# Performance work log

Hardware: AMD Instinct MI355X
Metric: run time of the kernel (lower is better)

Reference implementation:

```python
import jax, jax.numpy as jnp
import numpy as np

H = 896          # hidden_size
S = H // 2       # split_size = 448
Q = 256          # quantisation
B = 16384        # batch (parallel sampling streams)


def setup_inputs() -> dict:
    key = jax.random.key(0)
    ks = jax.random.split(key, 16)
    sc = 0.02
    return {
        "prev_y": jax.random.uniform(ks[0], (B, 2), dtype=jnp.float32),
        "prev_hidden": jax.random.normal(ks[1], (B, H), dtype=jnp.float32),
        "current_coarse": jax.random.uniform(ks[2], (B, 1), dtype=jnp.float32),
        # torch Linear weights are [out_features, in_features]
        "R_w": sc * jax.random.normal(ks[3], (3 * H, H), dtype=jnp.float32),
        "Ic_w": sc * jax.random.normal(ks[4], (3 * S, 2), dtype=jnp.float32),
        "If_w": sc * jax.random.normal(ks[5], (3 * S, 3), dtype=jnp.float32),
        "bias_u": jnp.zeros((H,), jnp.float32),
        "bias_r": jnp.zeros((H,), jnp.float32),
        "bias_e": jnp.zeros((H,), jnp.float32),
        "O1_w": sc * jax.random.normal(ks[6], (S, S), dtype=jnp.float32),
        "O1_b": jnp.zeros((S,), jnp.float32),
        "O2_w": sc * jax.random.normal(ks[7], (Q, S), dtype=jnp.float32),
        "O2_b": jnp.zeros((Q,), jnp.float32),
        "O3_w": sc * jax.random.normal(ks[8], (S, S), dtype=jnp.float32),
        "O3_b": jnp.zeros((S,), jnp.float32),
        "O4_w": sc * jax.random.normal(ks[9], (Q, S), dtype=jnp.float32),
        "O4_b": jnp.zeros((Q,), jnp.float32),
    }


def reference(prev_y, prev_hidden, current_coarse,
              R_w, Ic_w, If_w, bias_u, bias_r, bias_e,
              O1_w, O1_b, O2_w, O2_b, O3_w, O3_b, O4_w, O4_b):
    # recurrent projection: [B,H] @ [H,3H] -> [B,3H]
    R_hidden = prev_hidden @ R_w.T
    R_u, R_r, R_e = jnp.split(R_hidden, 3, axis=1)

    # coarse input projection: [B,2] -> [B,3S]
    cproj = prev_y @ Ic_w.T
    Ic_u, Ic_r, Ic_e = jnp.split(cproj, 3, axis=1)

    # fine input projection: [B,3] -> [B,3S]
    fine_in = jnp.concatenate([prev_y, current_coarse], axis=1)
    fproj = fine_in @ If_w.T
    If_u, If_r, If_e = jnp.split(fproj, 3, axis=1)

    I_u = jnp.concatenate([Ic_u, If_u], axis=1)  # [B,H]
    I_r = jnp.concatenate([Ic_r, If_r], axis=1)
    I_e = jnp.concatenate([Ic_e, If_e], axis=1)

    u = jax.nn.sigmoid(R_u + I_u + bias_u)
    r = jax.nn.sigmoid(R_r + I_r + bias_r)
    e = jnp.tanh(r * R_e + I_e + bias_e)
    hidden = u * prev_hidden + (1.0 - u) * e  # [B,H]

    h_coarse, h_fine = jnp.split(hidden, 2, axis=1)  # [B,S] each
    out_coarse = jax.nn.relu(h_coarse @ O1_w.T + O1_b) @ O2_w.T + O2_b  # [B,Q]
    out_fine = jax.nn.relu(h_fine @ O3_w.T + O3_b) @ O4_w.T + O4_b      # [B,Q]
    return (out_coarse, out_fine, hidden)
```

## Files before the change

kernel.cpp:

```cpp
#include <hip/hip_runtime.h>
#include <hip/hip_bf16.h>
#include <cstdint>

#define BB 16384
#define HH 896
#define SS 448
#define QQ 256
#define NPAD 2816

typedef __attribute__((ext_vector_type(4))) float f32x4;
typedef __attribute__((ext_vector_type(8))) short bf16x8;

__device__ __forceinline__ short f2bf(float f){
  union { float f; uint32_t u; } x; x.f = f;
  uint32_t r = (x.u + 0x7fffu + ((x.u >> 16) & 1u)) >> 16;
  return (short)r;
}
__device__ __forceinline__ float bf2f(short b){
  union { uint32_t u; float f; } x; x.u = ((uint32_t)(uint16_t)b) << 16;
  return x.f;
}

__global__ __launch_bounds__(256)
void castall_kernel(const float* __restrict__ ph, short* __restrict__ Ah,
                    const float* __restrict__ Rw, short* __restrict__ Rwh,
                    const float* __restrict__ O1w, short* __restrict__ O1b,
                    const float* __restrict__ O3w, short* __restrict__ O3b,
                    const float* __restrict__ O2w, short* __restrict__ O2b,
                    const float* __restrict__ O4w, short* __restrict__ O4b)
{
  int u = blockIdx.x * 256 + threadIdx.x;
  auto cp4 = [](short* d, const float* s, int jd, int js){
    float4 v = reinterpret_cast<const float4*>(s)[js];
    short4 o; o.x = f2bf(v.x); o.y = f2bf(v.y); o.z = f2bf(v.z); o.w = f2bf(v.w);
    reinterpret_cast<short4*>(d)[jd] = o;
  };
  auto z4 = [](short* d, int jd){
    short4 o; o.x = 0; o.y = 0; o.z = 0; o.w = 0;
    reinterpret_cast<short4*>(d)[jd] = o;
  };
  if (u < 3670016) { cp4(Ah, ph, u, u); return; }
  u -= 3670016;
  if (u < 602112) { cp4(Rwh, Rw, u, u); return; }
  u -= 602112;
  if (u < 28672) { z4(Rwh, 602112 + u); return; }
  u -= 28672;
  if (u < 57344) { if (u < 50176) cp4(O1b, O1w, u, u); else z4(O1b, u); return; }
  u -= 57344;
  if (u < 57344) { if (u < 50176) cp4(O3b, O3w, u, u); else z4(O3b, u); return; }
  u -= 57344;
  if (u < 32768) {
    int r = u >> 7, c4 = u & 127;
    if (c4 < 112) cp4(O2b, O2w, u, r * 112 + c4); else z4(O2b, u);
    return;
  }
  u -= 32768;
  if (u < 32768) {
    int r = u >> 7, c4 = u & 127;
    if (c4 < 112) cp4(O4b, O4w, u, r * 112 + c4); else z4(O4b, u);
    return;
  }
}

template<int EP>
__global__ __launch_bounds__(512, 2)
void gemm256_bt(const short* __restrict__ A0p, const short* __restrict__ A1p, int lda,
                const short* __restrict__ B0p, const short* __restrict__ B1p, int ldb,
                void* __restrict__ C0p, void* __restrict__ C1p, int ldc,
                const float* __restrict__ bias0, const float* __restrict__ bias1, int nbias,
                int Nvalid, int K, int nbn)
{
  const short* A  = blockIdx.z ? A1p : A0p;
  const short* Bt = blockIdx.z ? B1p : B0p;
  void* Cv        = blockIdx.z ? C1p : C0p;
  const float* bias = blockIdx.z ? bias1 : bias0;

  __shared__ short smem[65536];
  const int tid = threadIdx.x;
  const int w  = tid >> 6, ln = tid & 63;
  const int wr = w >> 2,  wc = w & 3;
  const int lr = ln & 15;
  const int lg = ln >> 4;
  const int srow = ln >> 3;
  const int sgc  = (ln & 7) ^ srow;

  int wg = blockIdx.x;
  const int cpx = gridDim.x >> 3;
  wg = (wg & 7) * cpx + (wg >> 3);
  const int bm = wg / nbn, bn = wg - bm * nbn;
  const long m0 = (long)bm * 256, n0 = (long)bn * 256;

  f32x4 acc[8][4] = {};

  auto stage = [&](const short* __restrict__ src, int ld, long rbase, int k0,
                   int lbase , int h) {
#pragma unroll
    for (int i = 0; i < 2; ++i) {
      const int rloc = h * 128 + i * 64 + w * 8;
      const short* g = src + (rbase + rloc + srow) * (long)ld + k0 + sgc * 8;
      __builtin_amdgcn_global_load_lds(
          (const __attribute__((address_space(1))) void*)g,
          (__attribute__((address_space(3))) void*)&smem[lbase + rloc * 64],
          16, 0, 0);
    }
  };
  auto rd = [&](int lbase, int r, int ks) -> bf16x8 {
    const int gc = ks * 4 + lg;
    return *reinterpret_cast<const bf16x8*>(&smem[lbase + r * 64 + ((gc ^ (r & 7)) << 3)]);
  };

  const int NT = K >> 6;
  stage(A,  lda, m0, 0, 0,     0);
  stage(Bt, ldb, n0, 0, 32768, 0);
  stage(Bt, ldb, n0, 0, 32768, 1);
  stage(A,  lda, m0, 0, 0,     1);
  asm volatile("s_waitcnt vmcnt(2)" ::: "memory");
  __builtin_amdgcn_s_barrier();
  asm volatile("" ::: "memory");
  __builtin_amdgcn_sched_barrier(0);

  for (int j = 0; j < NT; ++j) {
    const int Ab = (j & 1) * 16384;
    const int Bb = 32768 + (j & 1) * 16384;
    const int An = ((j + 1) & 1) * 16384;
    const int Bn = 32768 + ((j + 1) & 1) * 16384;
    const bool pf = (j + 1 < NT);
    const int k1 = (j + 1) << 6;
    bf16x8 b[4][2];
#pragma unroll
    for (int q = 0; q < 4; ++q) {
      bf16x8 a[2][2];
#pragma unroll
      for (int dm = 0; dm < 2; ++dm)
#pragma unroll
        for (int ks = 0; ks < 2; ++ks)
          a[dm][ks] = rd(Ab, q * 64 + dm * 32 + wr * 16 + lr, ks);
      if (q == 0) {
#pragma unroll
        for (int n = 0; n < 4; ++n)
#pragma unroll
          for (int ks = 0; ks < 2; ++ks)
            b[n][ks] = rd(Bb, wc * 64 + n * 16 + lr, ks);
        if (pf) {
          stage(A,  lda, m0, k1, An, 0);
          stage(Bt, ldb, n0, k1, Bn, 0);
          stage(Bt, ldb, n0, k1, Bn, 1);
          stage(A,  lda, m0, k1, An, 1);
        }
      }
      asm volatile("s_waitcnt lgkmcnt(0)" ::: "memory");
      __builtin_amdgcn_sched_barrier(0);
      __builtin_amdgcn_s_setprio(1);
#pragma unroll
      for (int dm = 0; dm < 2; ++dm)
#pragma unroll
        for (int n = 0; n < 4; ++n)
#pragma unroll
          for (int ks = 0; ks < 2; ++ks)
            acc[2 * q + dm][n] = __builtin_amdgcn_mfma_f32_16x16x32_bf16(
                a[dm][ks], b[n][ks], acc[2 * q + dm][n], 0, 0, 0);
      __builtin_amdgcn_s_setprio(0);
      __builtin_amdgcn_sched_barrier(0);
      if (q == 1) {
        if (pf) asm volatile("s_waitcnt vmcnt(8)" ::: "memory");
        else    asm volatile("s_waitcnt vmcnt(0)" ::: "memory");
        __builtin_amdgcn_s_barrier();
        asm volatile("" ::: "memory");
        __builtin_amdgcn_sched_barrier(0);
      } else if (q == 3) {
        asm volatile("s_waitcnt vmcnt(2)" ::: "memory");
        __builtin_amdgcn_s_barrier();
        asm volatile("" ::: "memory");
        __builtin_amdgcn_sched_barrier(0);
      }
    }
  }

  if (EP == 2) {
    const int lc = ln & 15, rg = lg * 4;
#pragma unroll
    for (int n = 0; n < 4; ++n) {
      const long col = n0 + wc * 64 + n * 16 + lc;
      const float bv = bias[col];
#pragma unroll
      for (int m = 0; m < 8; ++m) {
        const long row = m0 + m * 32 + wr * 16 + rg;
#pragma unroll
        for (int reg = 0; reg < 4; ++reg)
          ((float*)Cv)[(row + reg) * (long)ldc + col] = acc[m][n][reg] + bv;
      }
    }
    return;
  }

#pragma unroll
  for (int n = 0; n < 4; ++n) {
    const int col = wc * 64 + n * 16 + lr;
    float bv = 0.f;
    if (EP == 1) {
      const long gcol = n0 + col;
      bv = (gcol < nbias) ? bias[gcol] : 0.f;
    }
#pragma unroll
    for (int m = 0; m < 8; ++m) {
      const int row = m * 32 + wr * 16 + lg * 4;
#pragma unroll
      for (int reg = 0; reg < 4; ++reg) {
        float v = acc[m][n][reg];
        if (EP == 1) { v += bv; v = v > 0.f ? v : 0.f; }
        smem[(row + reg) * 256 + col] = f2bf(v);
      }
    }
  }
  __builtin_amdgcn_s_barrier();
  const int rt = tid >> 5;
  const int ct = (tid & 31) * 8;
  const long colg = n0 + ct;
  if (colg < Nvalid) {
#pragma unroll
    for (int p = 0; p < 16; ++p) {
      const int row = p * 16 + rt;
      bf16x8 v = *reinterpret_cast<const bf16x8*>(&smem[row * 256 + ct]);
      *reinterpret_cast<bf16x8*>(&((short*)Cv)[(m0 + row) * (long)ldc + colg]) = v;
    }
  }
}

__global__ __launch_bounds__(256)
void gates_kernel(const float* __restrict__ prev_y,
                  const short* __restrict__ Ah,
                  const float* __restrict__ ccoarse,
                  const float* __restrict__ Icw,
                  const float* __restrict__ Ifw,
                  const float* __restrict__ bu,
                  const float* __restrict__ br,
                  const float* __restrict__ be,
                  const short* __restrict__ Rh,
                  float* __restrict__ hid_out,
                  short* __restrict__ hid_bf)
{
  const int v = blockIdx.x * 256 + threadIdx.x;
  const int b = v / 112;
  const int h0 = (v - b * 112) * 8;
  const long rbase = (long)b * (3 * HH);

  const bf16x8 ru8 = *reinterpret_cast<const bf16x8*>(Rh + rbase + h0);
  const bf16x8 rr8 = *reinterpret_cast<const bf16x8*>(Rh + rbase + HH + h0);
  const bf16x8 re8 = *reinterpret_cast<const bf16x8*>(Rh + rbase + 2 * HH + h0);
  const bf16x8 ah8 = *reinterpret_cast<const bf16x8*>(Ah + (long)b * HH + h0);
  const float py0 = prev_y[2 * b], py1 = prev_y[2 * b + 1], c0 = ccoarse[b];

  float iu[8], ir[8], ie[8];
  if (h0 < SS) {
    const float4* cu = reinterpret_cast<const float4*>(Icw + 2 * h0);
    const float4* cr = reinterpret_cast<const float4*>(Icw + 2 * (SS + h0));
    const float4* ce = reinterpret_cast<const float4*>(Icw + 2 * (2 * SS + h0));
#pragma unroll
    for (int q = 0; q < 4; ++q) {
      float4 a = cu[q]; iu[2*q] = py0*a.x + py1*a.y; iu[2*q+1] = py0*a.z + py1*a.w;
      float4 r = cr[q]; ir[2*q] = py0*r.x + py1*r.y; ir[2*q+1] = py0*r.z + py1*r.w;
      float4 e = ce[q]; ie[2*q] = py0*e.x + py1*e.y; ie[2*q+1] = py0*e.z + py1*e.w;
    }
  } else {
    const int j0 = h0 - SS;
    const float* fu = Ifw + 3 * j0;
    const float* fr = Ifw + 3 * (SS + j0);
    const float* fe = Ifw + 3 * (2 * SS + j0);
#pragma unroll
    for (int j = 0; j < 8; ++j) {
      iu[j] = py0 * fu[3*j] + py1 * fu[3*j+1] + c0 * fu[3*j+2];
      ir[j] = py0 * fr[3*j] + py1 * fr[3*j+1] + c0 * fr[3*j+2];
      ie[j] = py0 * fe[3*j] + py1 * fe[3*j+1] + c0 * fe[3*j+2];
    }
  }
  const float4* bu4 = reinterpret_cast<const float4*>(bu + h0);
  const float4* br4 = reinterpret_cast<const float4*>(br + h0);
  const float4* be4 = reinterpret_cast<const float4*>(be + h0);
  float buv[8], brv[8], bev[8];
  { float4 a = bu4[0], b2 = bu4[1];
    buv[0]=a.x; buv[1]=a.y; buv[2]=a.z; buv[3]=a.w; buv[4]=b2.x; buv[5]=b2.y; buv[6]=b2.z; buv[7]=b2.w; }
  { float4 a = br4[0], b2 = br4[1];
    brv[0]=a.x; brv[1]=a.y; brv[2]=a.z; brv[3]=a.w; brv[4]=b2.x; brv[5]=b2.y; brv[6]=b2.z; brv[7]=b2.w; }
  { float4 a = be4[0], b2 = be4[1];
    bev[0]=a.x; bev[1]=a.y; bev[2]=a.z; bev[3]=a.w; bev[4]=b2.x; bev[5]=b2.y; bev[6]=b2.z; bev[7]=b2.w; }

  float hd[8];
  bf16x8 hb;
#pragma unroll
  for (int j = 0; j < 8; ++j) {
    float u = 1.f / (1.f + __expf(-(bf2f(ru8[j]) + iu[j] + buv[j])));
    float r = 1.f / (1.f + __expf(-(bf2f(rr8[j]) + ir[j] + brv[j])));
    float e = tanhf(r * bf2f(re8[j]) + ie[j] + bev[j]);
    hd[j] = u * bf2f(ah8[j]) + (1.f - u) * e;
    hb[j] = f2bf(hd[j]);
  }
  float4* ho = reinterpret_cast<float4*>(hid_out + (long)b * HH + h0);
  ho[0] = make_float4(hd[0], hd[1], hd[2], hd[3]);
  ho[1] = make_float4(hd[4], hd[5], hd[6], hd[7]);
  *reinterpret_cast<bf16x8*>(hid_bf + (long)b * HH + h0) = hb;
}

extern "C" void kernel_launch(void* const* d_in, const int* in_sizes, int n_in,
                              void* d_out, int out_size, void* d_ws, size_t ws_size,
                              hipStream_t stream)
{
  (void)in_sizes; (void)n_in; (void)out_size; (void)ws_size;
  const float* prev_y      = (const float*)d_in[0];
  const float* prev_hidden = (const float*)d_in[1];
  const float* ccoarse     = (const float*)d_in[2];
  const float* R_w  = (const float*)d_in[3];
  const float* Ic_w = (const float*)d_in[4];
  const float* If_w = (const float*)d_in[5];
  const float* bu   = (const float*)d_in[6];
  const float* br   = (const float*)d_in[7];
  const float* be   = (const float*)d_in[8];
  const float* O1w  = (const float*)d_in[9];
  const float* O1b  = (const float*)d_in[10];
  const float* O2w  = (const float*)d_in[11];
  const float* O2b  = (const float*)d_in[12];
  const float* O3w  = (const float*)d_in[13];
  const float* O3b  = (const float*)d_in[14];
  const float* O4w  = (const float*)d_in[15];
  const float* O4b  = (const float*)d_in[16];

  float* out_coarse = (float*)d_out;
  float* out_fine   = out_coarse + (long)BB * QQ;
  float* hidden     = out_fine + (long)BB * QQ;

  char* ws = (char*)d_ws;
  short* Ah   = (short*)(ws + 0);
  short* Rwh  = (short*)(ws + 29360128);
  short* Rh   = (short*)(ws + 34406400);
  short* hidb = (short*)(ws + 122486784);
  short* O1wb = (short*)(ws + 151846912);
  short* O3wb = (short*)(ws + 152305664);
  short* O2wb = (short*)(ws + 152764416);
  short* O4wb = (short*)(ws + 153026560);
  short* t1   = (short*)(ws + 0);
  short* t2   = (short*)(ws + 16777216);

  castall_kernel<<<17504, 256, 0, stream>>>(prev_hidden, Ah, R_w, Rwh,
                                            O1w, O1wb, O3w, O3wb, O2w, O2wb, O4w, O4wb);

  gemm256_bt<0><<<dim3(704, 1, 1), 512, 0, stream>>>(
      Ah, Ah, HH, Rwh, Rwh, HH, Rh, Rh, 3 * HH,
      nullptr, nullptr, 0, 3 * HH, HH, NPAD / 256);

  gates_kernel<<<BB * 112 / 256, 256, 0, stream>>>(prev_y, Ah, ccoarse,
                                                   Ic_w, If_w, bu, br, be, Rh, hidden, hidb);

  gemm256_bt<1><<<dim3(128, 1, 2), 512, 0, stream>>>(
      hidb, hidb + 448, HH, O1wb, O3wb, 448, t1, t2, 512,
      O1b, O3b, 448, 512, 448, 2);

  gemm256_bt<2><<<dim3(64, 1, 2), 512, 0, stream>>>(
      t1, t2, 512, O2wb, O4wb, 512, out_coarse, out_fine, QQ,
      O2b, O4b, QQ, QQ, 512, 1);
}
```

Measured before the change: 214.8 us.

## Restructure GEMM main loop into two phases and swizzle epilogue LDS staging

```diff
diff --git a/kernel.cpp b/kernel.cpp
--- a/kernel.cpp
+++ b/kernel.cpp
@@ -117,7 +117,6 @@
   asm volatile("s_waitcnt vmcnt(2)" ::: "memory");
   __builtin_amdgcn_s_barrier();
   asm volatile("" ::: "memory");
-  __builtin_amdgcn_sched_barrier(0);
 
   for (int j = 0; j < NT; ++j) {
     const int Ab = (j & 1) * 16384;
@@ -127,53 +126,68 @@
     const bool pf = (j + 1 < NT);
     const int k1 = (j + 1) << 6;
     bf16x8 b[4][2];
-#pragma unroll
-    for (int q = 0; q < 4; ++q) {
-      bf16x8 a[2][2];
-#pragma unroll
-      for (int dm = 0; dm < 2; ++dm)
+
+    __builtin_amdgcn_s_setprio(1);
+    {
+#pragma unroll
+      for (int n = 0; n < 4; ++n)
 #pragma unroll
         for (int ks = 0; ks < 2; ++ks)
-          a[dm][ks] = rd(Ab, q * 64 + dm * 32 + wr * 16 + lr, ks);
-      if (q == 0) {
-#pragma unroll
-        for (int n = 0; n < 4; ++n)
+          b[n][ks] = rd(Bb, wc * 64 + n * 16 + lr, ks);
+      if (pf) {
+        stage(A,  lda, m0, k1, An, 0);
+        stage(Bt, ldb, n0, k1, Bn, 0);
+        stage(Bt, ldb, n0, k1, Bn, 1);
+        stage(A,  lda, m0, k1, An, 1);
+      }
+#pragma unroll
+      for (int q = 0; q < 2; ++q) {
+        bf16x8 a[2][2];
+#pragma unroll
+        for (int dm = 0; dm < 2; ++dm)
 #pragma unroll
           for (int ks = 0; ks < 2; ++ks)
-            b[n][ks] = rd(Bb, wc * 64 + n * 16 + lr, ks);
-        if (pf) {
-          stage(A,  lda, m0, k1, An, 0);
-          stage(Bt, ldb, n0, k1, Bn, 0);
-          stage(Bt, ldb, n0, k1, Bn, 1);
-          stage(A,  lda, m0, k1, An, 1);
-        }
-      }
-      asm volatile("s_waitcnt lgkmcnt(0)" ::: "memory");
-      __builtin_amdgcn_sched_barrier(0);
-      __builtin_amdgcn_s_setprio(1);
-#pragma unroll
-      for (int dm = 0; dm < 2; ++dm)
-#pragma unroll
-        for (int n = 0; n < 4; ++n)
+            a[dm][ks] = rd(Ab, q * 64 + dm * 32 + wr * 16 + lr, ks);
+#pragma unroll
+        for (int dm = 0; dm < 2; ++dm)
+#pragma unroll
+          for (int n = 0; n < 4; ++n)
+#pragma unroll
+            for (int ks = 0; ks < 2; ++ks)
+              acc[2 * q + dm][n] = __builtin_amdgcn_mfma_f32_16x16x32_bf16(
+                  a[dm][ks], b[n][ks], acc[2 * q + dm][n], 0, 0, 0);
+      }
+    }
+    __builtin_amdgcn_s_setprio(0);
+    if (pf) asm volatile("s_waitcnt vmcnt(8)" ::: "memory");
+    else    asm volatile("s_waitcnt vmcnt(0)" ::: "memory");
+    __builtin_amdgcn_s_barrier();
+    asm volatile("" ::: "memory");
+
+    __builtin_amdgcn_s_setprio(1);
+    {
+#pragma unroll
+      for (int q = 2; q < 4; ++q) {
+        bf16x8 a[2][2];
+#pragma unroll
+        for (int dm = 0; dm < 2; ++dm)
 #pragma unroll
           for (int ks = 0; ks < 2; ++ks)
-            acc[2 * q + dm][n] = __builtin_amdgcn_mfma_f32_16x16x32_bf16(
-                a[dm][ks], b[n][ks], acc[2 * q + dm][n], 0, 0, 0);
-      __builtin_amdgcn_s_setprio(0);
-      __builtin_amdgcn_sched_barrier(0);
-      if (q == 1) {
-        if (pf) asm volatile("s_waitcnt vmcnt(8)" ::: "memory");
-        else    asm volatile("s_waitcnt vmcnt(0)" ::: "memory");
-        __builtin_amdgcn_s_barrier();
-        asm volatile("" ::: "memory");
-        __builtin_amdgcn_sched_barrier(0);
-      } else if (q == 3) {
-        asm volatile("s_waitcnt vmcnt(2)" ::: "memory");
-        __builtin_amdgcn_s_barrier();
-        asm volatile("" ::: "memory");
-        __builtin_amdgcn_sched_barrier(0);
-      }
-    }
+            a[dm][ks] = rd(Ab, q * 64 + dm * 32 + wr * 16 + lr, ks);
+#pragma unroll
+        for (int dm = 0; dm < 2; ++dm)
+#pragma unroll
+          for (int n = 0; n < 4; ++n)
+#pragma unroll
+            for (int ks = 0; ks < 2; ++ks)
+              acc[2 * q + dm][n] = __builtin_amdgcn_mfma_f32_16x16x32_bf16(
+                  a[dm][ks], b[n][ks], acc[2 * q + dm][n], 0, 0, 0);
+      }
+    }
+    __builtin_amdgcn_s_setprio(0);
+    asm volatile("s_waitcnt vmcnt(2)" ::: "memory");
+    __builtin_amdgcn_s_barrier();
+    asm volatile("" ::: "memory");
   }
 
   if (EP == 2) {
@@ -196,6 +210,7 @@
 #pragma unroll
   for (int n = 0; n < 4; ++n) {
     const int col = wc * 64 + n * 16 + lr;
+    const int gc = col >> 3, c7 = col & 7;
     float bv = 0.f;
     if (EP == 1) {
       const long gcol = n0 + col;
@@ -208,19 +223,21 @@
       for (int reg = 0; reg < 4; ++reg) {
         float v = acc[m][n][reg];
         if (EP == 1) { v += bv; v = v > 0.f ? v : 0.f; }
-        smem[(row + reg) * 256 + col] = f2bf(v);
+        const int rr = row + reg;
+        smem[rr * 256 + ((gc ^ ((rr >> 1) & 7)) << 3) + c7] = f2bf(v);
       }
     }
   }
   __builtin_amdgcn_s_barrier();
   const int rt = tid >> 5;
-  const int ct = (tid & 31) * 8;
-  const long colg = n0 + ct;
+  const int ctg = (tid & 31);
+  const long colg = n0 + ctg * 8;
   if (colg < Nvalid) {
 #pragma unroll
     for (int p = 0; p < 16; ++p) {
       const int row = p * 16 + rt;
-      bf16x8 v = *reinterpret_cast<const bf16x8*>(&smem[row * 256 + ct]);
+      bf16x8 v = *reinterpret_cast<const bf16x8*>(
+          &smem[row * 256 + ((ctg ^ ((row >> 1) & 7)) << 3)]);
       *reinterpret_cast<bf16x8*>(&((short*)Cv)[(m0 + row) * (long)ldc + colg]) = v;
     }
   }
```

New measurement: 215.4 us. Within noise of the previous version (+0.2%).

## Template GEMM on tile shape, use 4-wave blocks with BK=32, retile output GEMMs

Applied to the files above, without the earlier changes.

```diff
diff --git a/kernel.cpp b/kernel.cpp
--- a/kernel.cpp
+++ b/kernel.cpp
@@ -62,129 +62,111 @@
   }
 }
 
-template<int EP>
-__global__ __launch_bounds__(512, 2)
-void gemm256_bt(const short* __restrict__ A0p, const short* __restrict__ A1p, int lda,
-                const short* __restrict__ B0p, const short* __restrict__ B1p, int ldb,
-                void* __restrict__ C0p, void* __restrict__ C1p, int ldc,
-                const float* __restrict__ bias0, const float* __restrict__ bias1, int nbias,
-                int Nvalid, int K, int nbn)
+template<int EP, int BM, int BN>
+__global__ __launch_bounds__(256, 2)
+void gemm_t(const short* __restrict__ A0p, const short* __restrict__ A1p, int lda,
+            const short* __restrict__ B0p, const short* __restrict__ B1p, int ldb,
+            void* __restrict__ C0p, void* __restrict__ C1p, int ldc,
+            const float* __restrict__ bias0, const float* __restrict__ bias1, int nbias,
+            int Nvalid, int K, int nbn)
 {
+  constexpr int MF = BM / 32;
+  constexpr int NF = BN / 32;
+  constexpr int DB = (BM + BN) * 32;
+  __shared__ short smem[2 * DB];
+
   const short* A  = blockIdx.z ? A1p : A0p;
   const short* Bt = blockIdx.z ? B1p : B0p;
   void* Cv        = blockIdx.z ? C1p : C0p;
   const float* bias = blockIdx.z ? bias1 : bias0;
 
-  __shared__ short smem[65536];
   const int tid = threadIdx.x;
   const int w  = tid >> 6, ln = tid & 63;
-  const int wr = w >> 2,  wc = w & 3;
+  const int wr = w >> 1,  wc = w & 1;
   const int lr = ln & 15;
   const int lg = ln >> 4;
-  const int srow = ln >> 3;
-  const int sgc  = (ln & 7) ^ srow;
+  const int srow = ln >> 2;
+  const int sgc  = (ln & 3) ^ ((ln >> 3) & 3);
 
   int wg = blockIdx.x;
   const int cpx = gridDim.x >> 3;
   wg = (wg & 7) * cpx + (wg >> 3);
   const int bm = wg / nbn, bn = wg - bm * nbn;
-  const long m0 = (long)bm * 256, n0 = (long)bn * 256;
-
-  f32x4 acc[8][4] = {};
-
-  auto stage = [&](const short* __restrict__ src, int ld, long rbase, int k0,
-                   int lbase , int h) {
-#pragma unroll
-    for (int i = 0; i < 2; ++i) {
-      const int rloc = h * 128 + i * 64 + w * 8;
-      const short* g = src + (rbase + rloc + srow) * (long)ld + k0 + sgc * 8;
+  const long m0 = (long)bm * BM, n0 = (long)bn * BN;
+
+  f32x4 acc[MF][NF] = {};
+
+  auto stageA = [&](int k0, int base) {
+#pragma unroll
+    for (int i = 0; i < BM / 64; ++i) {
+      const int rloc = i * 64 + w * 16;
+      const short* g = A + (m0 + rloc + srow) * (long)lda + k0 + sgc * 8;
       __builtin_amdgcn_global_load_lds(
           (const __attribute__((address_space(1))) void*)g,
-          (__attribute__((address_space(3))) void*)&smem[lbase + rloc * 64],
+          (__attribute__((address_space(3))) void*)&smem[base + rloc * 32],
           16, 0, 0);
     }
   };
-  auto rd = [&](int lbase, int r, int ks) -> bf16x8 {
-    const int gc = ks * 4 + lg;
-    return *reinterpret_cast<const bf16x8*>(&smem[lbase + r * 64 + ((gc ^ (r & 7)) << 3)]);
-  };
-
-  const int NT = K >> 6;
-  stage(A,  lda, m0, 0, 0,     0);
-  stage(Bt, ldb, n0, 0, 32768, 0);
-  stage(Bt, ldb, n0, 0, 32768, 1);
-  stage(A,  lda, m0, 0, 0,     1);
-  asm volatile("s_waitcnt vmcnt(2)" ::: "memory");
+  auto stageB = [&](int k0, int base) {
+#pragma unroll
+    for (int i = 0; i < BN / 64; ++i) {
+      const int rloc = i * 64 + w * 16;
+      const short* g = Bt + (n0 + rloc + srow) * (long)ldb + k0 + sgc * 8;
+      __builtin_amdgcn_global_load_lds(
+          (const __attribute__((address_space(1))) void*)g,
+          (__attribute__((address_space(3))) void*)&smem[base + rloc * 32],
+          16, 0, 0);
+    }
+  };
+  auto rd = [&](int base, int r) -> bf16x8 {
+    return *reinterpret_cast<const bf16x8*>(
+        &smem[base + r * 32 + ((lg ^ ((r >> 1) & 3)) << 3)]);
+  };
+
+  const int NT = K >> 5;
+  stageA(0, 0);
+  stageB(0, BM * 32);
+  asm volatile("s_waitcnt vmcnt(0)" ::: "memory");
   __builtin_amdgcn_s_barrier();
   asm volatile("" ::: "memory");
-  __builtin_amdgcn_sched_barrier(0);
 
   for (int j = 0; j < NT; ++j) {
-    const int Ab = (j & 1) * 16384;
-    const int Bb = 32768 + (j & 1) * 16384;
-    const int An = ((j + 1) & 1) * 16384;
-    const int Bn = 32768 + ((j + 1) & 1) * 16384;
+    const int cur = (j & 1) * DB;
+    const int nxt = ((j + 1) & 1) * DB;
     const bool pf = (j + 1 < NT);
-    const int k1 = (j + 1) << 6;
-    bf16x8 b[4][2];
-#pragma unroll
-    for (int q = 0; q < 4; ++q) {
-      bf16x8 a[2][2];
-#pragma unroll
-      for (int dm = 0; dm < 2; ++dm)
-#pragma unroll
-        for (int ks = 0; ks < 2; ++ks)
-          a[dm][ks] = rd(Ab, q * 64 + dm * 32 + wr * 16 + lr, ks);
-      if (q == 0) {
-#pragma unroll
-        for (int n = 0; n < 4; ++n)
-#pragma unroll
-          for (int ks = 0; ks < 2; ++ks)
-            b[n][ks] = rd(Bb, wc * 64 + n * 16 + lr, ks);
-        if (pf) {
-          stage(A,  lda, m0, k1, An, 0);
-          stage(Bt, ldb, n0, k1, Bn, 0);
-          stage(Bt, ldb, n0, k1, Bn, 1);
-          stage(A,  lda, m0, k1, An, 1);
-        }
-      }
-      asm volatile("s_waitcnt lgkmcnt(0)" ::: "memory");
-      __builtin_amdgcn_sched_barrier(0);
-      __builtin_amdgcn_s_setprio(1);
-#pragma unroll
-      for (int dm = 0; dm < 2; ++dm)
-#pragma unroll
-        for (int n = 0; n < 4; ++n)
-#pragma unroll
-          for (int ks = 0; ks < 2; ++ks)
-            acc[2 * q + dm][n] = __builtin_amdgcn_mfma_f32_16x16x32_bf16(
-                a[dm][ks], b[n][ks], acc[2 * q + dm][n], 0, 0, 0);
-      __builtin_amdgcn_s_setprio(0);
-      __builtin_amdgcn_sched_barrier(0);
-      if (q == 1) {
-        if (pf) asm volatile("s_waitcnt vmcnt(8)" ::: "memory");
-        else    asm volatile("s_waitcnt vmcnt(0)" ::: "memory");
-        __builtin_amdgcn_s_barrier();
-        asm volatile("" ::: "memory");
-        __builtin_amdgcn_sched_barrier(0);
-      } else if (q == 3) {
-        asm volatile("s_waitcnt vmcnt(2)" ::: "memory");
-        __builtin_amdgcn_s_barrier();
-        asm volatile("" ::: "memory");
-        __builtin_amdgcn_sched_barrier(0);
-      }
-    }
+    const int k1 = (j + 1) << 5;
+    if (pf) { stageA(k1, nxt); stageB(k1, nxt + BM * 32); }
+
+    bf16x8 a[MF], b[NF];
+#pragma unroll
+    for (int n = 0; n < NF; ++n)
+      b[n] = rd(cur + BM * 32, wc * (BN / 2) + n * 16 + lr);
+#pragma unroll
+    for (int m = 0; m < MF; ++m)
+      a[m] = rd(cur, wr * (BM / 2) + m * 16 + lr);
+
+    __builtin_amdgcn_s_setprio(1);
+#pragma unroll
+    for (int m = 0; m < MF; ++m)
+#pragma unroll
+      for (int n = 0; n < NF; ++n)
+        acc[m][n] = __builtin_amdgcn_mfma_f32_16x16x32_bf16(a[m], b[n], acc[m][n], 0, 0, 0);
+    __builtin_amdgcn_s_setprio(0);
+
+    asm volatile("s_waitcnt vmcnt(0)" ::: "memory");
+    __builtin_amdgcn_s_barrier();
+    asm volatile("" ::: "memory");
   }
 
   if (EP == 2) {
-    const int lc = ln & 15, rg = lg * 4;
-#pragma unroll
-    for (int n = 0; n < 4; ++n) {
-      const long col = n0 + wc * 64 + n * 16 + lc;
+    const int rg = lg * 4;
+#pragma unroll
+    for (int n = 0; n < NF; ++n) {
+      const long col = n0 + wc * (BN / 2) + n * 16 + lr;
       const float bv = bias[col];
 #pragma unroll
-      for (int m = 0; m < 8; ++m) {
-        const long row = m0 + m * 32 + wr * 16 + rg;
+      for (int m = 0; m < MF; ++m) {
+        const long row = m0 + wr * (BM / 2) + m * 16 + rg;
 #pragma unroll
         for (int reg = 0; reg < 4; ++reg)
           ((float*)Cv)[(row + reg) * (long)ldc + col] = acc[m][n][reg] + bv;
@@ -194,35 +176,46 @@
   }
 
 #pragma unroll
-  for (int n = 0; n < 4; ++n) {
-    const int col = wc * 64 + n * 16 + lr;
-    float bv = 0.f;
-    if (EP == 1) {
-      const long gcol = n0 + col;
-      bv = (gcol < nbias) ? bias[gcol] : 0.f;
-    }
-#pragma unroll
-    for (int m = 0; m < 8; ++m) {
-      const int row = m * 32 + wr * 16 + lg * 4;
-#pragma unroll
-      for (int reg = 0; reg < 4; ++reg) {
-        float v = acc[m][n][reg];
-        if (EP == 1) { v += bv; v = v > 0.f ? v : 0.f; }
-        smem[(row + reg) * 256 + col] = f2bf(v);
+  for (int h = 0; h < 2; ++h) {
+    if (wr == h) {
+#pragma unroll
+      for (int n = 0; n < NF; ++n) {
+        const int col = wc * (BN / 2) + n * 16 + lr;
+        const int gc = col >> 3, c7 = col & 7;
+        float bv = 0.f;
+        if (EP == 1) {
+          const long gcol = n0 + col;
+          bv = (gcol < nbias) ? bias[gcol] : 0.f;
+        }
+#pragma unroll
+        for (int m = 0; m < MF; ++m) {
+#pragma unroll
+          for (int reg = 0; reg < 4; ++reg) {
+            float v = acc[m][n][reg];
+            if (EP == 1) { v += bv; v = v > 0.f ? v : 0.f; }
+            const int rl = m * 16 + lg * 4 + reg;
+            smem[rl * BN + ((gc ^ ((rl >> 1) & 7)) << 3) + c7] = f2bf(v);
+          }
+        }
       }
     }
-  }
-  __builtin_amdgcn_s_barrier();
-  const int rt = tid >> 5;
-  const int ct = (tid & 31) * 8;
-  const long colg = n0 + ct;
-  if (colg < Nvalid) {
-#pragma unroll
-    for (int p = 0; p < 16; ++p) {
-      const int row = p * 16 + rt;
-      bf16x8 v = *reinterpret_cast<const bf16x8*>(&smem[row * 256 + ct]);
-      *reinterpret_cast<bf16x8*>(&((short*)Cv)[(m0 + row) * (long)ldc + colg]) = v;
-    }
+    __builtin_amdgcn_s_barrier();
+    asm volatile("" ::: "memory");
+    const int rt = tid >> 5;
+    const int gcr = tid & 31;
+    const long colg = n0 + gcr * 8;
+    if (colg < Nvalid) {
+#pragma unroll
+      for (int p = 0; p < BM / 16; ++p) {
+        const int row = p * 8 + rt;
+        bf16x8 v = *reinterpret_cast<const bf16x8*>(
+            &smem[row * BN + ((gcr ^ ((row >> 1) & 7)) << 3)]);
+        *reinterpret_cast<bf16x8*>(
+            &((short*)Cv)[(m0 + h * (BM / 2) + row) * (long)ldc + colg]) = v;
+      }
+    }
+    __builtin_amdgcn_s_barrier();
+    asm volatile("" ::: "memory");
   }
 }
 
@@ -342,18 +335,18 @@
   castall_kernel<<<17504, 256, 0, stream>>>(prev_hidden, Ah, R_w, Rwh,
                                             O1w, O1wb, O3w, O3wb, O2w, O2wb, O4w, O4wb);
 
-  gemm256_bt<0><<<dim3(704, 1, 1), 512, 0, stream>>>(
+  gemm_t<0, 256, 256><<<dim3(704, 1, 1), 256, 0, stream>>>(
       Ah, Ah, HH, Rwh, Rwh, HH, Rh, Rh, 3 * HH,
-      nullptr, nullptr, 0, 3 * HH, HH, NPAD / 256);
+      nullptr, nullptr, 0, 3 * HH, HH, 11);
 
   gates_kernel<<<BB * 112 / 256, 256, 0, stream>>>(prev_y, Ah, ccoarse,
                                                    Ic_w, If_w, bu, br, be, Rh, hidden, hidb);
 
-  gemm256_bt<1><<<dim3(128, 1, 2), 512, 0, stream>>>(
+  gemm_t<1, 128, 256><<<dim3(256, 1, 2), 256, 0, stream>>>(
       hidb, hidb + 448, HH, O1wb, O3wb, 448, t1, t2, 512,
       O1b, O3b, 448, 512, 448, 2);
 
-  gemm256_bt<2><<<dim3(64, 1, 2), 512, 0, stream>>>(
+  gemm_t<2, 64, 256><<<dim3(256, 1, 2), 256, 0, stream>>>(
       t1, t2, 512, O2wb, O4wb, 512, out_coarse, out_fine, QQ,
       O2b, O4b, QQ, QQ, 512, 1);
 }
```

Result: slower. 842.6 us (+292.2%).
